# Kernel optimization log

Measured on AMD Instinct MI355X. Metric: run time of the kernel, lower is better.

The kernel has to match this reference:

```python
import jax, jax.numpy as jnp
import numpy as np

N = 50000
E = 1600000
INDIM, HIDIM, OUTDIM = 256, 128, 64


def setup_inputs() -> dict:
    key = jax.random.key(0)
    ks = jax.random.split(key, 4)
    x = jax.random.normal(ks[0], (N, INDIM), dtype=jnp.float32)
    edge_index = jax.random.randint(ks[1], (2, E), 0, N, dtype=jnp.int32)
    W1 = jax.random.normal(ks[2], (INDIM, HIDIM), dtype=jnp.float32) / np.float32(np.sqrt(INDIM))
    b1 = jnp.zeros((HIDIM,), dtype=jnp.float32)
    W2 = jax.random.normal(ks[3], (HIDIM, OUTDIM), dtype=jnp.float32) / np.float32(np.sqrt(HIDIM))
    b2 = jnp.zeros((OUTDIM,), dtype=jnp.float32)
    return {"x": x, "edge_index": edge_index, "W1": W1, "b1": b1, "W2": W2, "b2": b2}


def _gcn_conv(x, row, col, norm, W, b):
    # PyG GCNConv: transform first, then normalized scatter-add aggregation, then bias
    h = x @ W                              # [N, out]
    msg = h[row] * norm[:, None]           # gather source features, scale by edge norm
    out = jax.ops.segment_sum(msg, col, num_segments=x.shape[0])  # scatter-add to dst
    return out + b


def reference(x, edge_index, W1, b1, W2, b2):
    n = x.shape[0]
    # add self loops (PyG default add_self_loops=True)
    loops = jnp.arange(n, dtype=edge_index.dtype)
    row = jnp.concatenate([edge_index[0], loops])  # source nodes
    col = jnp.concatenate([edge_index[1], loops])  # destination nodes
    # symmetric normalization: deg^{-1/2}[row] * deg^{-1/2}[col], deg over dst incl. self loops
    deg = jax.ops.segment_sum(jnp.ones_like(col, dtype=x.dtype), col, num_segments=n)
    dinv = jnp.where(deg > 0, jax.lax.rsqrt(jnp.maximum(deg, 1.0)), 0.0)
    norm = dinv[row] * dinv[col]
    h = jax.nn.relu(_gcn_conv(x, row, col, norm, W1, b1))
    return _gcn_conv(h, row, col, norm, W2, b2)
```

## Files before the change

kernel.cpp:

```cpp
#include <hip/hip_runtime.h>

#define NN 50000
#define NE 1600000
#define INDIM 256
#define HIDIM 128
#define OUTDIM 64

#define NRANGE 128
#define RSPAN 400
#define ACAP 16384
#define NBBLK 1563
#define NDEG 256

typedef unsigned int uint;
typedef unsigned long long ull;
typedef unsigned short ushort;
typedef __attribute__((ext_vector_type(8))) short bf16x8;
typedef __attribute__((ext_vector_type(4))) float f32x4;

__device__ __forceinline__ ushort f2bf(float f) {
    uint u = __float_as_uint(f);
    uint r = (u + 0x7FFFu + ((u >> 16) & 1u)) >> 16;
    return (ushort)r;
}
__device__ __forceinline__ uint pk2(float a, float b) {
    return (uint)f2bf(a) | ((uint)f2bf(b) << 16);
}
__device__ __forceinline__ float bf_lo(uint u) { return __uint_as_float(u << 16); }
__device__ __forceinline__ float bf_hi(uint u) { return __uint_as_float(u & 0xFFFF0000u); }

#define ACC8(u) do { \
    a0 += bf_lo((u).x); a1 += bf_hi((u).x); \
    a2 += bf_lo((u).y); a3 += bf_hi((u).y); \
    a4 += bf_lo((u).z); a5 += bf_hi((u).z); \
    a6 += bf_lo((u).w); a7 += bf_hi((u).w); \
} while (0)


__global__ void k_wt(const float* __restrict__ W1, const float* __restrict__ W2,
                     ushort* __restrict__ W1T, ushort* __restrict__ W2T) {
    int idx = blockIdx.x * 256 + threadIdx.x;
    if (idx < INDIM * HIDIM) {
        int k = idx / HIDIM, nn = idx % HIDIM;
        W1T[nn * INDIM + k] = f2bf(W1[idx]);
    } else {
        int j = idx - INDIM * HIDIM;
        if (j < HIDIM * OUTDIM) {
            int k = j / OUTDIM, nn = j % OUTDIM;
            W2T[nn * HIDIM + k] = f2bf(W2[j]);
        }
    }
}


__global__ void k_bcnt(const int* __restrict__ col, int* __restrict__ bcnt) {
    __shared__ int bins[NRANGE];
    int tid = threadIdx.x;
    if (tid < NRANGE) bins[tid] = 0;
    __syncthreads();
    int base = blockIdx.x * 1024 + tid;
#pragma unroll
    for (int k = 0; k < 4; k++) {
        int i = base + k * 256;
        if (i < NE) atomicAdd(&bins[col[i] / RSPAN], 1);
    }
    __syncthreads();
    if (tid < NRANGE) bcnt[tid * NBBLK + blockIdx.x] = bins[tid];
}


__global__ void k_bscan(const int* __restrict__ bcnt, int* __restrict__ bbase,
                        int* __restrict__ rcur) {
    __shared__ int wsum[16];
    __shared__ int woff[16];
    int r = blockIdx.x;
    const int* src = bcnt + r * NBBLK;
    int* dst = bbase + r * NBBLK;
    int tid = threadIdx.x, lane = tid & 63, wid = tid >> 6;
    int seg = tid * 2;
    int l0 = (seg < NBBLK) ? src[seg] : 0;
    int l1 = (seg + 1 < NBBLK) ? src[seg + 1] : 0;
    int sum = l0 + l1;
    int incl = sum;
#pragma unroll
    for (int off = 1; off < 64; off <<= 1) {
        int t = __shfl_up(incl, off);
        if (lane >= off) incl += t;
    }
    if (lane == 63) wsum[wid] = incl;
    __syncthreads();
    if (wid == 0 && lane < 16) {
        int wv = wsum[lane];
        int wincl = wv;
#pragma unroll
        for (int off = 1; off < 16; off <<= 1) {
            int t = __shfl_up(wincl, off);
            if (lane >= off) wincl += t;
        }
        woff[lane] = wincl - wv;
    }
    __syncthreads();
    int run = incl - sum + woff[wid];
    if (seg < NBBLK) dst[seg] = run;
    if (seg + 1 < NBBLK) dst[seg + 1] = run + l0;
    if (tid == 1023) rcur[r] = run + sum;
}


__global__ void k_bscat(const int* __restrict__ row, const int* __restrict__ col,
                        const int* __restrict__ bbase, uint* __restrict__ staged) {
    __shared__ int cur[NRANGE];
    int tid = threadIdx.x;
    if (tid < NRANGE) cur[tid] = bbase[tid * NBBLK + blockIdx.x];
    __syncthreads();
    int base = blockIdx.x * 1024 + tid;
#pragma unroll
    for (int k = 0; k < 4; k++) {
        int i = base + k * 256;
        if (i < NE) {
            int d = col[i], s = row[i];
            int r = d / RSPAN;
            int off = atomicAdd(&cur[r], 1);
            staged[(size_t)r * ACAP + off] = ((uint)s << 10) | (uint)(d - r * RSPAN);
        }
    }
}


__global__ void k_sort(const uint* __restrict__ staged, const int* __restrict__ rcur,
                       float* __restrict__ dinv, float* __restrict__ dinv_p,
                       int* __restrict__ row_ptr_p, int* __restrict__ perm,
                       ushort* __restrict__ ssrc_p) {
    __shared__ int bins[RSPAN];
    __shared__ int pdeg[RSPAN];
    __shared__ int prow[RSPAN];
    __shared__ int lperm[RSPAN];
    __shared__ int dh[NDEG];
    __shared__ int wsum[16];
    __shared__ int woff[16];
    int r = blockIdx.x;
    int tid = threadIdx.x, lane = tid & 63, wid = tid >> 6;
    int lo = r * RSPAN;
    int count = rcur[r];
    int rbase = 0;
    for (int rr = 0; rr < r; rr++) rbase += rcur[rr];
    if (lo >= NN) {
        if (lo == NN && tid == 0) row_ptr_p[NN] = rbase;
        return;
    }
    const uint* st = staged + (size_t)r * ACAP;

    if (tid < RSPAN) bins[tid] = 0;
    if (tid < NDEG) dh[tid] = 0;
    __syncthreads();

    for (int i = tid; i < count; i += 1024)
        atomicAdd(&bins[st[i] & 1023u], 1);
    __syncthreads();

    int deg = (tid < RSPAN) ? bins[tid] : 0;
    bool valid = tid < RSPAN;
    if (valid) {
        dinv[lo + tid] = rsqrtf((float)(deg + 1));
        atomicAdd(&dh[min(deg, NDEG - 1)], 1);
    }
    __syncthreads();

    if (wid == 0) {
        int b = lane * 4;
        int v0 = dh[b], v1 = dh[b + 1], v2 = dh[b + 2], v3 = dh[b + 3];
        int s = v0 + v1 + v2 + v3;
        int incl = s;
#pragma unroll
        for (int off = 1; off < 64; off <<= 1) {
            int t = __shfl_up(incl, off);
            if (lane >= off) incl += t;
        }
        int excl = incl - s;
        dh[b] = excl;
        dh[b + 1] = excl + v0;
        dh[b + 2] = excl + v0 + v1;
        dh[b + 3] = excl + v0 + v1 + v2;
    }
    __syncthreads();

    int rl = 0;
    if (valid) rl = atomicAdd(&dh[min(deg, NDEG - 1)], 1);
    if (valid) { pdeg[rl] = deg; lperm[rl] = tid; }
    __syncthreads();

    int v = (tid < RSPAN) ? pdeg[tid] : 0;
    int incl = v;
#pragma unroll
    for (int off = 1; off < 64; off <<= 1) {
        int t = __shfl_up(incl, off);
        if (lane >= off) incl += t;
    }
    if (lane == 63) wsum[wid] = incl;
    __syncthreads();
    if (wid == 0 && lane < 16) {
        int wv = wsum[lane];
        int wincl = wv;
#pragma unroll
        for (int off = 1; off < 16; off <<= 1) {
            int t = __shfl_up(wincl, off);
            if (lane >= off) wincl += t;
        }
        woff[lane] = wincl - wv;
    }
    __syncthreads();
    int excl = incl - v + woff[wid];
    if (tid < RSPAN) prow[tid] = excl;
    __syncthreads();

    if (tid < RSPAN) {
        int di = lo + tid;
        row_ptr_p[di] = rbase + prow[tid];
        perm[di] = lo + lperm[tid];
        dinv_p[di] = rsqrtf((float)(pdeg[tid] + 1));
    }
    __syncthreads();
    if (valid) bins[tid] = rbase + prow[rl];
    __syncthreads();

    for (int i = tid; i < count; i += 1024) {
        uint rec = st[i];
        int pos = atomicAdd(&bins[rec & 1023u], 1);
        ssrc_p[pos] = (ushort)(rec >> 10);
    }
}


__global__ void k_gemm1(const float* __restrict__ A, const ushort* __restrict__ W1T,
                        const float* __restrict__ dinv, ushort* __restrict__ g1s, int n) {
    __shared__ ushort As[64 * 40];
    __shared__ ushort Bs[128 * 40];
    int tid = threadIdx.x;
    int w = tid >> 6, lane = tid & 63;
    int ln = lane & 15, quad = lane >> 4;
    int row0 = blockIdx.x * 64;
    int n0 = w * 32;

    f32x4 acc[4][2];
#pragma unroll
    for (int m = 0; m < 4; m++)
#pragma unroll
        for (int t = 0; t < 2; t++) acc[m][t] = (f32x4){0.f, 0.f, 0.f, 0.f};

    int ar = tid >> 2;
    int ac = (tid & 3) * 8;

    for (int k0 = 0; k0 < INDIM; k0 += 32) {
        {
            int gr = row0 + ar;
            uint4 u = make_uint4(0, 0, 0, 0);
            if (gr < n) {
                const float* p = A + (size_t)gr * INDIM + k0 + ac;
                float4 v0 = *(const float4*)p;
                float4 v1 = *(const float4*)(p + 4);
                u.x = pk2(v0.x, v0.y); u.y = pk2(v0.z, v0.w);
                u.z = pk2(v1.x, v1.y); u.w = pk2(v1.z, v1.w);
            }
            *(uint4*)(As + ar * 40 + ac) = u;
        }
#pragma unroll
        for (int it = 0; it < 2; it++) {
            int idx = tid + it * 256;
            int bn = idx >> 2, bc = (idx & 3) * 8;
            uint4 u = *(const uint4*)(W1T + (size_t)bn * INDIM + k0 + bc);
            *(uint4*)(Bs + bn * 40 + bc) = u;
        }
        __syncthreads();

        bf16x8 af[4], bf[2];
#pragma unroll
        for (int m = 0; m < 4; m++)
            af[m] = *(const bf16x8*)(As + (m * 16 + ln) * 40 + quad * 8);
#pragma unroll
        for (int t = 0; t < 2; t++)
            bf[t] = *(const bf16x8*)(Bs + (n0 + t * 16 + ln) * 40 + quad * 8);
#pragma unroll
        for (int m = 0; m < 4; m++)
#pragma unroll
            for (int t = 0; t < 2; t++)
                acc[m][t] = __builtin_amdgcn_mfma_f32_16x16x32_bf16(af[m], bf[t], acc[m][t], 0, 0, 0);
        __syncthreads();
    }

    int slice = w >> 1;
    int fbase = (w & 1) * 32;
#pragma unroll
    for (int m = 0; m < 4; m++) {
#pragma unroll
        for (int r = 0; r < 4; r++) {
            int gr = row0 + m * 16 + quad * 4 + r;
            if (gr < n) {
                float dv = dinv[gr];
#pragma unroll
                for (int t = 0; t < 2; t++) {
                    int cj = t * 16 + ln;
                    g1s[((size_t)slice * NN + gr) * 64 + fbase + cj] = f2bf(acc[m][t][r] * dv);
                }
            }
        }
    }
}


__global__ void k_agg1(const ushort* __restrict__ g1s, const float* __restrict__ dinv_p,
                       const int* __restrict__ row_ptr_p, const ushort* __restrict__ ssrc_p,
                       const int* __restrict__ perm, const float* __restrict__ b1,
                       ushort* __restrict__ hrb) {
    int slice = blockIdx.x & 1;
    int dbase = (blockIdx.x >> 1) * 32;
    int wid = threadIdx.x >> 6, lane = threadIdx.x & 63;
    int grp = lane >> 3, fl = lane & 7;
    int di = dbase + wid * 8 + grp;
    if (di >= NN) return;
    int d = perm[di];
    const ushort* gs = g1s + (size_t)slice * NN * 64 + fl * 8;
    float a0 = 0.f, a1 = 0.f, a2 = 0.f, a3 = 0.f;
    float a4 = 0.f, a5 = 0.f, a6 = 0.f, a7 = 0.f;
    int e0 = row_ptr_p[di], e1 = row_ptr_p[di + 1];
    if (e1 > e0) {
        int last = e1 - 1;
        int sB0 = ssrc_p[min(e0 + 0, last)];
        int sB1 = ssrc_p[min(e0 + 1, last)];
        int sB2 = ssrc_p[min(e0 + 2, last)];
        int sB3 = ssrc_p[min(e0 + 3, last)];
        uint4 uA0 = *(const uint4*)(gs + (size_t)sB0 * 64);
        uint4 uA1 = *(const uint4*)(gs + (size_t)sB1 * 64);
        uint4 uA2 = *(const uint4*)(gs + (size_t)sB2 * 64);
        uint4 uA3 = *(const uint4*)(gs + (size_t)sB3 * 64);
        sB0 = ssrc_p[min(e0 + 4, last)];
        sB1 = ssrc_p[min(e0 + 5, last)];
        sB2 = ssrc_p[min(e0 + 6, last)];
        sB3 = ssrc_p[min(e0 + 7, last)];
        for (int eb = e0; eb < e1; eb += 4) {
            int p0 = ssrc_p[min(eb + 8, last)];
            int p1 = ssrc_p[min(eb + 9, last)];
            int p2 = ssrc_p[min(eb + 10, last)];
            int p3 = ssrc_p[min(eb + 11, last)];
            uint4 v0 = *(const uint4*)(gs + (size_t)sB0 * 64);
            uint4 v1 = *(const uint4*)(gs + (size_t)sB1 * 64);
            uint4 v2 = *(const uint4*)(gs + (size_t)sB2 * 64);
            uint4 v3 = *(const uint4*)(gs + (size_t)sB3 * 64);
            uint4 z = make_uint4(0u, 0u, 0u, 0u);
            if (eb + 1 >= e1) uA1 = z;
            if (eb + 2 >= e1) uA2 = z;
            if (eb + 3 >= e1) uA3 = z;
            ACC8(uA0); ACC8(uA1); ACC8(uA2); ACC8(uA3);
            uA0 = v0; uA1 = v1; uA2 = v2; uA3 = v3;
            sB0 = p0; sB1 = p1; sB2 = p2; sB3 = p3;
        }
    }
    uint4 ud = *(const uint4*)(gs + (size_t)d * 64);
    ACC8(ud);
    float dv = dinv_p[di];
    const float* bp = b1 + slice * 64 + fl * 8;
    float4 bb0 = *(const float4*)bp;
    float4 bb1 = *(const float4*)(bp + 4);
    uint4 o;
    o.x = pk2(fmaxf(a0 * dv + bb0.x, 0.f), fmaxf(a1 * dv + bb0.y, 0.f));
    o.y = pk2(fmaxf(a2 * dv + bb0.z, 0.f), fmaxf(a3 * dv + bb0.w, 0.f));
    o.z = pk2(fmaxf(a4 * dv + bb1.x, 0.f), fmaxf(a5 * dv + bb1.y, 0.f));
    o.w = pk2(fmaxf(a6 * dv + bb1.z, 0.f), fmaxf(a7 * dv + bb1.w, 0.f));
    *(uint4*)(hrb + ((size_t)slice * NN + di) * 64 + fl * 8) = o;
}


__global__ void k_gemm2(const ushort* __restrict__ hrb, const ushort* __restrict__ W2T,
                        const float* __restrict__ dinv_p, const int* __restrict__ perm,
                        ushort* __restrict__ g2s, int n) {
    __shared__ ushort As[64 * 40];
    __shared__ ushort Bs[64 * 40];
    int tid = threadIdx.x;
    int w = tid >> 6, lane = tid & 63;
    int ln = lane & 15, quad = lane >> 4;
    int row0 = blockIdx.x * 64;
    int n0 = w * 16;

    f32x4 acc[4];
#pragma unroll
    for (int m = 0; m < 4; m++) acc[m] = (f32x4){0.f, 0.f, 0.f, 0.f};

    int ar = tid >> 2;
    int ac = (tid & 3) * 8;

    for (int k0 = 0; k0 < HIDIM; k0 += 32) {
        {
            int gr = row0 + ar;
            uint4 u = make_uint4(0, 0, 0, 0);
            if (gr < n) u = *(const uint4*)(hrb + ((size_t)(k0 >> 6) * NN + gr) * 64 + (k0 & 63) + ac);
            *(uint4*)(As + ar * 40 + ac) = u;
        }
        {
            int bn = tid >> 2, bc = (tid & 3) * 8;
            uint4 u = *(const uint4*)(W2T + (size_t)bn * HIDIM + k0 + bc);
            *(uint4*)(Bs + bn * 40 + bc) = u;
        }
        __syncthreads();

        bf16x8 bf = *(const bf16x8*)(Bs + (n0 + ln) * 40 + quad * 8);
#pragma unroll
        for (int m = 0; m < 4; m++) {
            bf16x8 af = *(const bf16x8*)(As + (m * 16 + ln) * 40 + quad * 8);
            acc[m] = __builtin_amdgcn_mfma_f32_16x16x32_bf16(af, bf, acc[m], 0, 0, 0);
        }
        __syncthreads();
    }

    int col = n0 + ln;
#pragma unroll
    for (int m = 0; m < 4; m++) {
#pragma unroll
        for (int r = 0; r < 4; r++) {
            int gr = row0 + m * 16 + quad * 4 + r;
            if (gr < n) {
                int gd = perm[gr];
                g2s[(size_t)gd * 64 + col] = f2bf(acc[m][r] * dinv_p[gr]);
            }
        }
    }
}


__global__ void k_agg2(const ushort* __restrict__ g2s, const float* __restrict__ dinv_p,
                       const int* __restrict__ row_ptr_p, const ushort* __restrict__ ssrc_p,
                       const int* __restrict__ perm, const float* __restrict__ b2,
                       float* __restrict__ out) {
    int dbase = blockIdx.x * 32;
    int wid = threadIdx.x >> 6, lane = threadIdx.x & 63;
    int grp = lane >> 3, fl = lane & 7;
    int di = dbase + wid * 8 + grp;
    if (di >= NN) return;
    int d = perm[di];
    const ushort* gs = g2s + fl * 8;
    float a0 = 0.f, a1 = 0.f, a2 = 0.f, a3 = 0.f;
    float a4 = 0.f, a5 = 0.f, a6 = 0.f, a7 = 0.f;
    int e0 = row_ptr_p[di], e1 = row_ptr_p[di + 1];
    if (e1 > e0) {
        int last = e1 - 1;
        int sB0 = ssrc_p[min(e0 + 0, last)];
        int sB1 = ssrc_p[min(e0 + 1, last)];
        int sB2 = ssrc_p[min(e0 + 2, last)];
        int sB3 = ssrc_p[min(e0 + 3, last)];
        uint4 uA0 = *(const uint4*)(gs + (size_t)sB0 * 64);
        uint4 uA1 = *(const uint4*)(gs + (size_t)sB1 * 64);
        uint4 uA2 = *(const uint4*)(gs + (size_t)sB2 * 64);
        uint4 uA3 = *(const uint4*)(gs + (size_t)sB3 * 64);
        sB0 = ssrc_p[min(e0 + 4, last)];
        sB1 = ssrc_p[min(e0 + 5, last)];
        sB2 = ssrc_p[min(e0 + 6, last)];
        sB3 = ssrc_p[min(e0 + 7, last)];
        for (int eb = e0; eb < e1; eb += 4) {
            int p0 = ssrc_p[min(eb + 8, last)];
            int p1 = ssrc_p[min(eb + 9, last)];
            int p2 = ssrc_p[min(eb + 10, last)];
            int p3 = ssrc_p[min(eb + 11, last)];
            uint4 v0 = *(const uint4*)(gs + (size_t)sB0 * 64);
            uint4 v1 = *(const uint4*)(gs + (size_t)sB1 * 64);
            uint4 v2 = *(const uint4*)(gs + (size_t)sB2 * 64);
            uint4 v3 = *(const uint4*)(gs + (size_t)sB3 * 64);
            uint4 z = make_uint4(0u, 0u, 0u, 0u);
            if (eb + 1 >= e1) uA1 = z;
            if (eb + 2 >= e1) uA2 = z;
            if (eb + 3 >= e1) uA3 = z;
            ACC8(uA0); ACC8(uA1); ACC8(uA2); ACC8(uA3);
            uA0 = v0; uA1 = v1; uA2 = v2; uA3 = v3;
            sB0 = p0; sB1 = p1; sB2 = p2; sB3 = p3;
        }
    }
    uint4 ud = *(const uint4*)(gs + (size_t)d * 64);
    ACC8(ud);
    float dv = dinv_p[di];
    const float* bp = b2 + fl * 8;
    float4 bb0 = *(const float4*)bp;
    float4 bb1 = *(const float4*)(bp + 4);
    float4 r0, r1;
    r0.x = a0 * dv + bb0.x;
    r0.y = a1 * dv + bb0.y;
    r0.z = a2 * dv + bb0.z;
    r0.w = a3 * dv + bb0.w;
    r1.x = a4 * dv + bb1.x;
    r1.y = a5 * dv + bb1.y;
    r1.z = a6 * dv + bb1.z;
    r1.w = a7 * dv + bb1.w;
    float* op = out + (size_t)d * OUTDIM + fl * 8;
    *(float4*)op = r0;
    *(float4*)(op + 4) = r1;
}


extern "C" void kernel_launch(void* const* d_in, const int* in_sizes, int n_in,
                              void* d_out, int out_size, void* d_ws, size_t ws_size,
                              hipStream_t stream) {
    const float* x   = (const float*)d_in[0];
    const int*   ei  = (const int*)d_in[1];
    const float* W1  = (const float*)d_in[2];
    const float* b1  = (const float*)d_in[3];
    const float* W2  = (const float*)d_in[4];
    const float* b2  = (const float*)d_in[5];
    float* out = (float*)d_out;

    const int* row = ei;
    const int* col = ei + NE;

    size_t off = 0;
    auto alloc = [&](size_t bytes) {
        void* p = (char*)d_ws + off;
        off += (bytes + 255) & ~(size_t)255;
        return p;
    };
    float*  dinv     = (float*) alloc((size_t)NN * 4);
    int*    rcur     = (int*)   alloc(NRANGE * 4);
    int*    bcnt     = (int*)   alloc((size_t)NRANGE * NBBLK * 4);
    int*    bbase    = (int*)   alloc((size_t)NRANGE * NBBLK * 4);
    uint*   staged   = (uint*)  alloc((size_t)NRANGE * ACAP * 4);
    ushort* ssrc_p   = (ushort*)alloc((size_t)NE * 2);
    ushort* W1T      = (ushort*)alloc((size_t)INDIM * HIDIM * 2);
    ushort* W2T      = (ushort*)alloc((size_t)HIDIM * OUTDIM * 2);
    ushort* g1s      = (ushort*)alloc((size_t)NN * HIDIM * 2);
    ushort* hrb      = (ushort*)alloc((size_t)NN * HIDIM * 2);
    ushort* g2s      = (ushort*)alloc((size_t)NN * OUTDIM * 2);
    int*    perm     = (int*)   alloc((size_t)NN * 4);
    int*    row_ptr_p= (int*)   alloc((size_t)(NN + 1) * 4);
    float*  dinv_p   = (float*) alloc((size_t)NN * 4);

    const int nb32 = (NN + 31) / 32;
    const int nb64 = (NN + 63) / 64;

    k_wt<<<(INDIM * HIDIM + HIDIM * OUTDIM + 255) / 256, 256, 0, stream>>>(W1, W2, W1T, W2T);

    k_bcnt<<<NBBLK, 256, 0, stream>>>(col, bcnt);
    k_bscan<<<NRANGE, 1024, 0, stream>>>(bcnt, bbase, rcur);
    k_bscat<<<NBBLK, 256, 0, stream>>>(row, col, bbase, staged);

    k_sort<<<NRANGE, 1024, 0, stream>>>(staged, rcur, dinv, dinv_p, row_ptr_p, perm, ssrc_p);

    k_gemm1<<<nb64, 256, 0, stream>>>(x, W1T, dinv, g1s, NN);
    k_agg1<<<nb32 * 2, 256, 0, stream>>>(g1s, dinv_p, row_ptr_p, ssrc_p, perm, b1, hrb);
    k_gemm2<<<nb64, 256, 0, stream>>>(hrb, W2T, dinv_p, perm, g2s, NN);
    k_agg2<<<nb32, 256, 0, stream>>>(g2s, dinv_p, row_ptr_p, ssrc_p, perm, b2, out);
}
```

Measured before the change: 217.2 us.

## Overlap bucket sort with GEMM1 and split features into 32-wide slices

Computes degrees with global atomics during bucket counting so dinv is ready early, then merges the per-range sort and the first GEMM into one launch where extra blocks run GEMM1 alongside the sort blocks. The feature layouts for g1s, hrb and g2s are re-sliced into 32-column planes, and both aggregation kernels now use 4 lanes per node per slice, giving more, smaller gathers that touch a narrower working set. This adds global atomics on deg, 1024-thread GEMM blocks with more shared memory, and more redundant index reads per slice.

```diff
diff --git a/kernel.cpp b/kernel.cpp
--- a/kernel.cpp
+++ b/kernel.cpp
@@ -11,6 +11,7 @@
 #define ACAP 16384
 #define NBBLK 1563
 #define NDEG 256
+#define NG1 196
 
 typedef unsigned int uint;
 typedef unsigned long long ull;
@@ -38,8 +39,10 @@
 
 
 __global__ void k_wt(const float* __restrict__ W1, const float* __restrict__ W2,
-                     ushort* __restrict__ W1T, ushort* __restrict__ W2T) {
+                     ushort* __restrict__ W1T, ushort* __restrict__ W2T,
+                     int* __restrict__ deg) {
     int idx = blockIdx.x * 256 + threadIdx.x;
+    for (int i = idx; i < NN; i += gridDim.x * 256) deg[i] = 0;
     if (idx < INDIM * HIDIM) {
         int k = idx / HIDIM, nn = idx % HIDIM;
         W1T[nn * INDIM + k] = f2bf(W1[idx]);
@@ -53,7 +56,8 @@
 }
 
 
-__global__ void k_bcnt(const int* __restrict__ col, int* __restrict__ bcnt) {
+__global__ void k_bcnt(const int* __restrict__ col, int* __restrict__ bcnt,
+                       int* __restrict__ deg) {
     __shared__ int bins[NRANGE];
     int tid = threadIdx.x;
     if (tid < NRANGE) bins[tid] = 0;
@@ -62,7 +66,11 @@
 #pragma unroll
     for (int k = 0; k < 4; k++) {
         int i = base + k * 256;
-        if (i < NE) atomicAdd(&bins[col[i] / RSPAN], 1);
+        if (i < NE) {
+            int d = col[i];
+            atomicAdd(&bins[d / RSPAN], 1);
+            atomicAdd(&deg[d], 1);
+        }
     }
     __syncthreads();
     if (tid < NRANGE) bcnt[tid * NBBLK + blockIdx.x] = bins[tid];
@@ -70,13 +78,16 @@
 
 
 __global__ void k_bscan(const int* __restrict__ bcnt, int* __restrict__ bbase,
-                        int* __restrict__ rcur) {
+                        int* __restrict__ rcur, const int* __restrict__ deg,
+                        float* __restrict__ dinv) {
     __shared__ int wsum[16];
     __shared__ int woff[16];
     int r = blockIdx.x;
     const int* src = bcnt + r * NBBLK;
     int* dst = bbase + r * NBBLK;
     int tid = threadIdx.x, lane = tid & 63, wid = tid >> 6;
+    int gid = r * 1024 + tid;
+    if (gid < NN) dinv[gid] = rsqrtf((float)(deg[gid] + 1));
     int seg = tid * 2;
     int l0 = (seg < NBBLK) ? src[seg] : 0;
     int l1 = (seg + 1 < NBBLK) ? src[seg + 1] : 0;
@@ -127,10 +138,12 @@
 }
 
 
-__global__ void k_sort(const uint* __restrict__ staged, const int* __restrict__ rcur,
-                       float* __restrict__ dinv, float* __restrict__ dinv_p,
-                       int* __restrict__ row_ptr_p, int* __restrict__ perm,
-                       ushort* __restrict__ ssrc_p) {
+__global__ __launch_bounds__(1024) void k_sg1(
+        const uint* __restrict__ staged, const int* __restrict__ rcur,
+        float* __restrict__ dinv_p, int* __restrict__ row_ptr_p,
+        int* __restrict__ perm, ushort* __restrict__ ssrc_p,
+        const float* __restrict__ A, const ushort* __restrict__ W1T,
+        const float* __restrict__ dinv, ushort* __restrict__ g1s, int n) {
     __shared__ int bins[RSPAN];
     __shared__ int pdeg[RSPAN];
     __shared__ int prow[RSPAN];
@@ -138,168 +151,165 @@
     __shared__ int dh[NDEG];
     __shared__ int wsum[16];
     __shared__ int woff[16];
-    int r = blockIdx.x;
+    __shared__ ushort As[4 * 64 * 40];
+    __shared__ ushort Bs[128 * 40];
+
     int tid = threadIdx.x, lane = tid & 63, wid = tid >> 6;
-    int lo = r * RSPAN;
-    int count = rcur[r];
-    int rbase = 0;
-    for (int rr = 0; rr < r; rr++) rbase += rcur[rr];
-    if (lo >= NN) {
-        if (lo == NN && tid == 0) row_ptr_p[NN] = rbase;
-        return;
-    }
-    const uint* st = staged + (size_t)r * ACAP;
-
-    if (tid < RSPAN) bins[tid] = 0;
-    if (tid < NDEG) dh[tid] = 0;
-    __syncthreads();
-
-    for (int i = tid; i < count; i += 1024)
-        atomicAdd(&bins[st[i] & 1023u], 1);
-    __syncthreads();
-
-    int deg = (tid < RSPAN) ? bins[tid] : 0;
-    bool valid = tid < RSPAN;
-    if (valid) {
-        dinv[lo + tid] = rsqrtf((float)(deg + 1));
-        atomicAdd(&dh[min(deg, NDEG - 1)], 1);
-    }
-    __syncthreads();
-
-    if (wid == 0) {
-        int b = lane * 4;
-        int v0 = dh[b], v1 = dh[b + 1], v2 = dh[b + 2], v3 = dh[b + 3];
-        int s = v0 + v1 + v2 + v3;
-        int incl = s;
+
+    if (blockIdx.x < NRANGE) {
+        int r = blockIdx.x;
+        int lo = r * RSPAN;
+        int count = rcur[r];
+        int rbase = 0;
+        for (int rr = 0; rr < r; rr++) rbase += rcur[rr];
+        if (lo >= NN) {
+            if (lo == NN && tid == 0) row_ptr_p[NN] = rbase;
+            return;
+        }
+        const uint* st = staged + (size_t)r * ACAP;
+
+        if (tid < RSPAN) bins[tid] = 0;
+        if (tid < NDEG) dh[tid] = 0;
+        __syncthreads();
+
+        for (int i = tid; i < count; i += 1024)
+            atomicAdd(&bins[st[i] & 1023u], 1);
+        __syncthreads();
+
+        int deg = (tid < RSPAN) ? bins[tid] : 0;
+        bool valid = tid < RSPAN;
+        if (valid) atomicAdd(&dh[min(deg, NDEG - 1)], 1);
+        __syncthreads();
+
+        if (wid == 0) {
+            int b = lane * 4;
+            int v0 = dh[b], v1 = dh[b + 1], v2 = dh[b + 2], v3 = dh[b + 3];
+            int s = v0 + v1 + v2 + v3;
+            int incl = s;
+#pragma unroll
+            for (int off = 1; off < 64; off <<= 1) {
+                int t = __shfl_up(incl, off);
+                if (lane >= off) incl += t;
+            }
+            int excl = incl - s;
+            dh[b] = excl;
+            dh[b + 1] = excl + v0;
+            dh[b + 2] = excl + v0 + v1;
+            dh[b + 3] = excl + v0 + v1 + v2;
+        }
+        __syncthreads();
+
+        int rl = 0;
+        if (valid) rl = atomicAdd(&dh[min(deg, NDEG - 1)], 1);
+        if (valid) { pdeg[rl] = deg; lperm[rl] = tid; }
+        __syncthreads();
+
+        int v = (tid < RSPAN) ? pdeg[tid] : 0;
+        int incl = v;
 #pragma unroll
         for (int off = 1; off < 64; off <<= 1) {
             int t = __shfl_up(incl, off);
             if (lane >= off) incl += t;
         }
-        int excl = incl - s;
-        dh[b] = excl;
-        dh[b + 1] = excl + v0;
-        dh[b + 2] = excl + v0 + v1;
-        dh[b + 3] = excl + v0 + v1 + v2;
-    }
-    __syncthreads();
-
-    int rl = 0;
-    if (valid) rl = atomicAdd(&dh[min(deg, NDEG - 1)], 1);
-    if (valid) { pdeg[rl] = deg; lperm[rl] = tid; }
-    __syncthreads();
-
-    int v = (tid < RSPAN) ? pdeg[tid] : 0;
-    int incl = v;
-#pragma unroll
-    for (int off = 1; off < 64; off <<= 1) {
-        int t = __shfl_up(incl, off);
-        if (lane >= off) incl += t;
-    }
-    if (lane == 63) wsum[wid] = incl;
-    __syncthreads();
-    if (wid == 0 && lane < 16) {
-        int wv = wsum[lane];
-        int wincl = wv;
-#pragma unroll
-        for (int off = 1; off < 16; off <<= 1) {
-            int t = __shfl_up(wincl, off);
-            if (lane >= off) wincl += t;
-        }
-        woff[lane] = wincl - wv;
-    }
-    __syncthreads();
-    int excl = incl - v + woff[wid];
-    if (tid < RSPAN) prow[tid] = excl;
-    __syncthreads();
-
-    if (tid < RSPAN) {
-        int di = lo + tid;
-        row_ptr_p[di] = rbase + prow[tid];
-        perm[di] = lo + lperm[tid];
-        dinv_p[di] = rsqrtf((float)(pdeg[tid] + 1));
-    }
-    __syncthreads();
-    if (valid) bins[tid] = rbase + prow[rl];
-    __syncthreads();
-
-    for (int i = tid; i < count; i += 1024) {
-        uint rec = st[i];
-        int pos = atomicAdd(&bins[rec & 1023u], 1);
-        ssrc_p[pos] = (ushort)(rec >> 10);
-    }
-}
-
-
-__global__ void k_gemm1(const float* __restrict__ A, const ushort* __restrict__ W1T,
-                        const float* __restrict__ dinv, ushort* __restrict__ g1s, int n) {
-    __shared__ ushort As[64 * 40];
-    __shared__ ushort Bs[128 * 40];
-    int tid = threadIdx.x;
-    int w = tid >> 6, lane = tid & 63;
-    int ln = lane & 15, quad = lane >> 4;
-    int row0 = blockIdx.x * 64;
-    int n0 = w * 32;
-
-    f32x4 acc[4][2];
-#pragma unroll
-    for (int m = 0; m < 4; m++)
-#pragma unroll
-        for (int t = 0; t < 2; t++) acc[m][t] = (f32x4){0.f, 0.f, 0.f, 0.f};
-
-    int ar = tid >> 2;
-    int ac = (tid & 3) * 8;
-
-    for (int k0 = 0; k0 < INDIM; k0 += 32) {
-        {
-            int gr = row0 + ar;
-            uint4 u = make_uint4(0, 0, 0, 0);
-            if (gr < n) {
-                const float* p = A + (size_t)gr * INDIM + k0 + ac;
-                float4 v0 = *(const float4*)p;
-                float4 v1 = *(const float4*)(p + 4);
-                u.x = pk2(v0.x, v0.y); u.y = pk2(v0.z, v0.w);
-                u.z = pk2(v1.x, v1.y); u.w = pk2(v1.z, v1.w);
+        if (lane == 63) wsum[wid] = incl;
+        __syncthreads();
+        if (wid == 0 && lane < 16) {
+            int wv = wsum[lane];
+            int wincl = wv;
+#pragma unroll
+            for (int off = 1; off < 16; off <<= 1) {
+                int t = __shfl_up(wincl, off);
+                if (lane >= off) wincl += t;
             }
-            *(uint4*)(As + ar * 40 + ac) = u;
-        }
-#pragma unroll
-        for (int it = 0; it < 2; it++) {
-            int idx = tid + it * 256;
-            int bn = idx >> 2, bc = (idx & 3) * 8;
-            uint4 u = *(const uint4*)(W1T + (size_t)bn * INDIM + k0 + bc);
-            *(uint4*)(Bs + bn * 40 + bc) = u;
-        }
-        __syncthreads();
-
-        bf16x8 af[4], bf[2];
+            woff[lane] = wincl - wv;
+        }
+        __syncthreads();
+        int excl = incl - v + woff[wid];
+        if (tid < RSPAN) prow[tid] = excl;
+        __syncthreads();
+
+        if (tid < RSPAN) {
+            int di = lo + tid;
+            row_ptr_p[di] = rbase + prow[tid];
+            perm[di] = lo + lperm[tid];
+            dinv_p[di] = rsqrtf((float)(pdeg[tid] + 1));
+        }
+        __syncthreads();
+        if (valid) bins[tid] = rbase + prow[rl];
+        __syncthreads();
+
+        for (int i = tid; i < count; i += 1024) {
+            uint rec = st[i];
+            int pos = atomicAdd(&bins[rec & 1023u], 1);
+            ssrc_p[pos] = (ushort)(rec >> 10);
+        }
+    } else {
+        int sub = blockIdx.x - NRANGE;
+        int g = tid >> 8;
+        int t256 = tid & 255;
+        int w = t256 >> 6;
+        int l256 = t256 & 63;
+        int ln = l256 & 15, quad = l256 >> 4;
+        int row0 = (sub * 4 + g) * 64;
+        int n0 = w * 32;
+        ushort* Asg = As + g * (64 * 40);
+
+        f32x4 acc[4][2];
 #pragma unroll
         for (int m = 0; m < 4; m++)
-            af[m] = *(const bf16x8*)(As + (m * 16 + ln) * 40 + quad * 8);
-#pragma unroll
-        for (int t = 0; t < 2; t++)
-            bf[t] = *(const bf16x8*)(Bs + (n0 + t * 16 + ln) * 40 + quad * 8);
-#pragma unroll
-        for (int m = 0; m < 4; m++)
+#pragma unroll
+            for (int t = 0; t < 2; t++) acc[m][t] = (f32x4){0.f, 0.f, 0.f, 0.f};
+
+        int ar = t256 >> 2;
+        int ac = (t256 & 3) * 8;
+
+        for (int k0 = 0; k0 < INDIM; k0 += 32) {
+            {
+                int gr = row0 + ar;
+                uint4 u = make_uint4(0, 0, 0, 0);
+                if (gr < n) {
+                    const float* p = A + (size_t)gr * INDIM + k0 + ac;
+                    float4 v0 = *(const float4*)p;
+                    float4 v1 = *(const float4*)(p + 4);
+                    u.x = pk2(v0.x, v0.y); u.y = pk2(v0.z, v0.w);
+                    u.z = pk2(v1.x, v1.y); u.w = pk2(v1.z, v1.w);
+                }
+                *(uint4*)(Asg + ar * 40 + ac) = u;
+            }
+            if (tid < 512) {
+                int bn = tid >> 2, bc = (tid & 3) * 8;
+                uint4 u = *(const uint4*)(W1T + (size_t)bn * INDIM + k0 + bc);
+                *(uint4*)(Bs + bn * 40 + bc) = u;
+            }
+            __syncthreads();
+
+            bf16x8 af[4], bf[2];
+#pragma unroll
+            for (int m = 0; m < 4; m++)
+                af[m] = *(const bf16x8*)(Asg + (m * 16 + ln) * 40 + quad * 8);
 #pragma unroll
             for (int t = 0; t < 2; t++)
-                acc[m][t] = __builtin_amdgcn_mfma_f32_16x16x32_bf16(af[m], bf[t], acc[m][t], 0, 0, 0);
-        __syncthreads();
-    }
-
-    int slice = w >> 1;
-    int fbase = (w & 1) * 32;
-#pragma unroll
-    for (int m = 0; m < 4; m++) {
-#pragma unroll
-        for (int r = 0; r < 4; r++) {
-            int gr = row0 + m * 16 + quad * 4 + r;
-            if (gr < n) {
-                float dv = dinv[gr];
-#pragma unroll
-                for (int t = 0; t < 2; t++) {
-                    int cj = t * 16 + ln;
-                    g1s[((size_t)slice * NN + gr) * 64 + fbase + cj] = f2bf(acc[m][t][r] * dv);
+                bf[t] = *(const bf16x8*)(Bs + (n0 + t * 16 + ln) * 40 + quad * 8);
+#pragma unroll
+            for (int m = 0; m < 4; m++)
+#pragma unroll
+                for (int t = 0; t < 2; t++)
+                    acc[m][t] = __builtin_amdgcn_mfma_f32_16x16x32_bf16(af[m], bf[t], acc[m][t], 0, 0, 0);
+            __syncthreads();
+        }
+
+#pragma unroll
+        for (int m = 0; m < 4; m++) {
+#pragma unroll
+            for (int r2 = 0; r2 < 4; r2++) {
+                int gr = row0 + m * 16 + quad * 4 + r2;
+                if (gr < n) {
+                    float dv = dinv[gr];
+#pragma unroll
+                    for (int t = 0; t < 2; t++) {
+                        int cj = t * 16 + ln;
+                        g1s[((size_t)w * NN + gr) * 32 + cj] = f2bf(acc[m][t][r2] * dv);
+                    }
                 }
             }
         }
@@ -311,14 +321,14 @@
                        const int* __restrict__ row_ptr_p, const ushort* __restrict__ ssrc_p,
                        const int* __restrict__ perm, const float* __restrict__ b1,
                        ushort* __restrict__ hrb) {
-    int slice = blockIdx.x & 1;
-    int dbase = (blockIdx.x >> 1) * 32;
+    int slice = (blockIdx.x & 7) >> 1;
+    int dbase = (blockIdx.x >> 3) * 64;
     int wid = threadIdx.x >> 6, lane = threadIdx.x & 63;
-    int grp = lane >> 3, fl = lane & 7;
-    int di = dbase + wid * 8 + grp;
+    int grp = lane >> 2, fl = lane & 3;
+    int di = dbase + wid * 16 + grp;
     if (di >= NN) return;
     int d = perm[di];
-    const ushort* gs = g1s + (size_t)slice * NN * 64 + fl * 8;
+    const ushort* gs = g1s + (size_t)slice * NN * 32 + fl * 8;
     float a0 = 0.f, a1 = 0.f, a2 = 0.f, a3 = 0.f;
     float a4 = 0.f, a5 = 0.f, a6 = 0.f, a7 = 0.f;
     int e0 = row_ptr_p[di], e1 = row_ptr_p[di + 1];
@@ -328,10 +338,10 @@
         int sB1 = ssrc_p[min(e0 + 1, last)];
         int sB2 = ssrc_p[min(e0 + 2, last)];
         int sB3 = ssrc_p[min(e0 + 3, last)];
-        uint4 uA0 = *(const uint4*)(gs + (size_t)sB0 * 64);
-        uint4 uA1 = *(const uint4*)(gs + (size_t)sB1 * 64);
-        uint4 uA2 = *(const uint4*)(gs + (size_t)sB2 * 64);
-        uint4 uA3 = *(const uint4*)(gs + (size_t)sB3 * 64);
+        uint4 uA0 = *(const uint4*)(gs + (size_t)sB0 * 32);
+        uint4 uA1 = *(const uint4*)(gs + (size_t)sB1 * 32);
+        uint4 uA2 = *(const uint4*)(gs + (size_t)sB2 * 32);
+        uint4 uA3 = *(const uint4*)(gs + (size_t)sB3 * 32);
         sB0 = ssrc_p[min(e0 + 4, last)];
         sB1 = ssrc_p[min(e0 + 5, last)];
         sB2 = ssrc_p[min(e0 + 6, last)];
@@ -341,10 +351,10 @@
             int p1 = ssrc_p[min(eb + 9, last)];
             int p2 = ssrc_p[min(eb + 10, last)];
             int p3 = ssrc_p[min(eb + 11, last)];
-            uint4 v0 = *(const uint4*)(gs + (size_t)sB0 * 64);
-            uint4 v1 = *(const uint4*)(gs + (size_t)sB1 * 64);
-            uint4 v2 = *(const uint4*)(gs + (size_t)sB2 * 64);
-            uint4 v3 = *(const uint4*)(gs + (size_t)sB3 * 64);
+            uint4 v0 = *(const uint4*)(gs + (size_t)sB0 * 32);
+            uint4 v1 = *(const uint4*)(gs + (size_t)sB1 * 32);
+            uint4 v2 = *(const uint4*)(gs + (size_t)sB2 * 32);
+            uint4 v3 = *(const uint4*)(gs + (size_t)sB3 * 32);
             uint4 z = make_uint4(0u, 0u, 0u, 0u);
             if (eb + 1 >= e1) uA1 = z;
             if (eb + 2 >= e1) uA2 = z;
@@ -354,10 +364,10 @@
             sB0 = p0; sB1 = p1; sB2 = p2; sB3 = p3;
         }
     }
-    uint4 ud = *(const uint4*)(gs + (size_t)d * 64);
+    uint4 ud = *(const uint4*)(gs + (size_t)d * 32);
     ACC8(ud);
     float dv = dinv_p[di];
-    const float* bp = b1 + slice * 64 + fl * 8;
+    const float* bp = b1 + slice * 32 + fl * 8;
     float4 bb0 = *(const float4*)bp;
     float4 bb1 = *(const float4*)(bp + 4);
     uint4 o;
@@ -365,7 +375,7 @@
     o.y = pk2(fmaxf(a2 * dv + bb0.z, 0.f), fmaxf(a3 * dv + bb0.w, 0.f));
     o.z = pk2(fmaxf(a4 * dv + bb1.x, 0.f), fmaxf(a5 * dv + bb1.y, 0.f));
     o.w = pk2(fmaxf(a6 * dv + bb1.z, 0.f), fmaxf(a7 * dv + bb1.w, 0.f));
-    *(uint4*)(hrb + ((size_t)slice * NN + di) * 64 + fl * 8) = o;
+    *(uint4*)(hrb + ((size_t)slice * NN + di) * 32 + fl * 8) = o;
 }
 
 
@@ -388,10 +398,11 @@
     int ac = (tid & 3) * 8;
 
     for (int k0 = 0; k0 < HIDIM; k0 += 32) {
+        int hs = k0 >> 5;
         {
             int gr = row0 + ar;
             uint4 u = make_uint4(0, 0, 0, 0);
-            if (gr < n) u = *(const uint4*)(hrb + ((size_t)(k0 >> 6) * NN + gr) * 64 + (k0 & 63) + ac);
+            if (gr < n) u = *(const uint4*)(hrb + ((size_t)hs * NN + gr) * 32 + ac);
             *(uint4*)(As + ar * 40 + ac) = u;
         }
         {
@@ -411,6 +422,7 @@
     }
 
     int col = n0 + ln;
+    int s2 = col >> 5, cj = col & 31;
 #pragma unroll
     for (int m = 0; m < 4; m++) {
 #pragma unroll
@@ -418,7 +430,7 @@
             int gr = row0 + m * 16 + quad * 4 + r;
             if (gr < n) {
                 int gd = perm[gr];
-                g2s[(size_t)gd * 64 + col] = f2bf(acc[m][r] * dinv_p[gr]);
+                g2s[((size_t)s2 * NN + gd) * 32 + cj] = f2bf(acc[m][r] * dinv_p[gr]);
             }
         }
     }
@@ -429,13 +441,14 @@
                        const int* __restrict__ row_ptr_p, const ushort* __restrict__ ssrc_p,
                        const int* __restrict__ perm, const float* __restrict__ b2,
                        float* __restrict__ out) {
-    int dbase = blockIdx.x * 32;
+    int slice = (blockIdx.x & 7) >> 2;
+    int dbase = (blockIdx.x >> 3) * 64;
     int wid = threadIdx.x >> 6, lane = threadIdx.x & 63;
-    int grp = lane >> 3, fl = lane & 7;
-    int di = dbase + wid * 8 + grp;
+    int grp = lane >> 2, fl = lane & 3;
+    int di = dbase + wid * 16 + grp;
     if (di >= NN) return;
     int d = perm[di];
-    const ushort* gs = g2s + fl * 8;
+    const ushort* gs = g2s + (size_t)slice * NN * 32 + fl * 8;
     float a0 = 0.f, a1 = 0.f, a2 = 0.f, a3 = 0.f;
     float a4 = 0.f, a5 = 0.f, a6 = 0.f, a7 = 0.f;
     int e0 = row_ptr_p[di], e1 = row_ptr_p[di + 1];
@@ -445,10 +458,10 @@
         int sB1 = ssrc_p[min(e0 + 1, last)];
         int sB2 = ssrc_p[min(e0 + 2, last)];
         int sB3 = ssrc_p[min(e0 + 3, last)];
-        uint4 uA0 = *(const uint4*)(gs + (size_t)sB0 * 64);
-        uint4 uA1 = *(const uint4*)(gs + (size_t)sB1 * 64);
-        uint4 uA2 = *(const uint4*)(gs + (size_t)sB2 * 64);
-        uint4 uA3 = *(const uint4*)(gs + (size_t)sB3 * 64);
+        uint4 uA0 = *(const uint4*)(gs + (size_t)sB0 * 32);
+        uint4 uA1 = *(const uint4*)(gs + (size_t)sB1 * 32);
+        uint4 uA2 = *(const uint4*)(gs + (size_t)sB2 * 32);
+        uint4 uA3 = *(const uint4*)(gs + (size_t)sB3 * 32);
         sB0 = ssrc_p[min(e0 + 4, last)];
         sB1 = ssrc_p[min(e0 + 5, last)];
         sB2 = ssrc_p[min(e0 + 6, last)];
@@ -458,10 +471,10 @@
             int p1 = ssrc_p[min(eb + 9, last)];
             int p2 = ssrc_p[min(eb + 10, last)];
             int p3 = ssrc_p[min(eb + 11, last)];
-            uint4 v0 = *(const uint4*)(gs + (size_t)sB0 * 64);
-            uint4 v1 = *(const uint4*)(gs + (size_t)sB1 * 64);
-            uint4 v2 = *(const uint4*)(gs + (size_t)sB2 * 64);
-            uint4 v3 = *(const uint4*)(gs + (size_t)sB3 * 64);
+            uint4 v0 = *(const uint4*)(gs + (size_t)sB0 * 32);
+            uint4 v1 = *(const uint4*)(gs + (size_t)sB1 * 32);
+            uint4 v2 = *(const uint4*)(gs + (size_t)sB2 * 32);
+            uint4 v3 = *(const uint4*)(gs + (size_t)sB3 * 32);
             uint4 z = make_uint4(0u, 0u, 0u, 0u);
             if (eb + 1 >= e1) uA1 = z;
             if (eb + 2 >= e1) uA2 = z;
@@ -471,10 +484,10 @@
             sB0 = p0; sB1 = p1; sB2 = p2; sB3 = p3;
         }
     }
-    uint4 ud = *(const uint4*)(gs + (size_t)d * 64);
+    uint4 ud = *(const uint4*)(gs + (size_t)d * 32);
     ACC8(ud);
     float dv = dinv_p[di];
-    const float* bp = b2 + fl * 8;
+    const float* bp = b2 + slice * 32 + fl * 8;
     float4 bb0 = *(const float4*)bp;
     float4 bb1 = *(const float4*)(bp + 4);
     float4 r0, r1;
@@ -486,7 +499,7 @@
     r1.y = a5 * dv + bb1.y;
     r1.z = a6 * dv + bb1.z;
     r1.w = a7 * dv + bb1.w;
-    float* op = out + (size_t)d * OUTDIM + fl * 8;
+    float* op = out + (size_t)d * OUTDIM + slice * 32 + fl * 8;
     *(float4*)op = r0;
     *(float4*)(op + 4) = r1;
 }
@@ -513,6 +526,7 @@
         return p;
     };
     float*  dinv     = (float*) alloc((size_t)NN * 4);
+    int*    deg      = (int*)   alloc((size_t)NN * 4);
     int*    rcur     = (int*)   alloc(NRANGE * 4);
     int*    bcnt     = (int*)   alloc((size_t)NRANGE * NBBLK * 4);
     int*    bbase    = (int*)   alloc((size_t)NRANGE * NBBLK * 4);
@@ -527,19 +541,18 @@
     int*    row_ptr_p= (int*)   alloc((size_t)(NN + 1) * 4);
     float*  dinv_p   = (float*) alloc((size_t)NN * 4);
 
-    const int nb32 = (NN + 31) / 32;
     const int nb64 = (NN + 63) / 64;
 
-    k_wt<<<(INDIM * HIDIM + HIDIM * OUTDIM + 255) / 256, 256, 0, stream>>>(W1, W2, W1T, W2T);
-
-    k_bcnt<<<NBBLK, 256, 0, stream>>>(col, bcnt);
-    k_bscan<<<NRANGE, 1024, 0, stream>>>(bcnt, bbase, rcur);
+    k_wt<<<(INDIM * HIDIM + HIDIM * OUTDIM + 255) / 256, 256, 0, stream>>>(W1, W2, W1T, W2T, deg);
+
+    k_bcnt<<<NBBLK, 256, 0, stream>>>(col, bcnt, deg);
+    k_bscan<<<NRANGE, 1024, 0, stream>>>(bcnt, bbase, rcur, deg, dinv);
     k_bscat<<<NBBLK, 256, 0, stream>>>(row, col, bbase, staged);
 
-    k_sort<<<NRANGE, 1024, 0, stream>>>(staged, rcur, dinv, dinv_p, row_ptr_p, perm, ssrc_p);
-
-    k_gemm1<<<nb64, 256, 0, stream>>>(x, W1T, dinv, g1s, NN);
-    k_agg1<<<nb32 * 2, 256, 0, stream>>>(g1s, dinv_p, row_ptr_p, ssrc_p, perm, b1, hrb);
+    k_sg1<<<NRANGE + NG1, 1024, 0, stream>>>(staged, rcur, dinv_p, row_ptr_p, perm, ssrc_p,
+                                             x, W1T, dinv, g1s, NN);
+
+    k_agg1<<<nb64 * 8, 256, 0, stream>>>(g1s, dinv_p, row_ptr_p, ssrc_p, perm, b1, hrb);
     k_gemm2<<<nb64, 256, 0, stream>>>(hrb, W2T, dinv_p, perm, g2s, NN);
-    k_agg2<<<nb32, 256, 0, stream>>>(g2s, dinv_p, row_ptr_p, ssrc_p, perm, b2, out);
-}
+    k_agg2<<<nb64 * 8, 256, 0, stream>>>(g2s, dinv_p, row_ptr_p, ssrc_p, perm, b2, out);
+}
```

Result: slower. 381.6 us (+75.7%).
